# Optimization experiments

Measured on AMD Instinct MI355X. Metric: run time of the kernel, lower is better.

The kernel has to match this reference:

```python
import jax, jax.numpy as jnp
import numpy as np


def _apply_rope(x, cos, sin):
    # x: [B, h, T, d]; cos/sin: [T, d//2]
    B, h, T, d = x.shape
    xp = x.astype(jnp.float32).reshape(B, h, T, d // 2, 2)
    xr, xi = xp[..., 0], xp[..., 1]
    c = cos[None, None]  # [1,1,T,d//2]
    s = sin[None, None]
    out_r = xr * c - xi * s
    out_i = xr * s + xi * c
    out = jnp.stack([out_r, out_i], axis=-1).reshape(B, h, T, d)
    return out.astype(x.dtype)


def setup_inputs() -> dict:
    key = jax.random.key(0)
    ks = jax.random.split(key, 7)
    B, T, C = 1, 4096, 1024
    h = 16
    d = C // h
    return {
        "x": jax.random.normal(ks[0], (B, T, C), jnp.float32),
        "freqs_cos": jax.random.normal(ks[1], (T, d // 2), jnp.float32),
        "freqs_sin": jax.random.normal(ks[2], (T, d // 2), jnp.float32),
        "Wq": jax.random.normal(ks[3], (C, C), jnp.float32) * 0.02,
        "Wk": jax.random.normal(ks[4], (C, C), jnp.float32) * 0.02,
        "Wv": jax.random.normal(ks[5], (C, C), jnp.float32) * 0.02,
        "Wo": jax.random.normal(ks[6], (C, C), jnp.float32) * 0.02,
    }


def reference(x, freqs_cos, freqs_sin, Wq, Wk, Wv, Wo):
    B, T, C = x.shape
    h = 16
    d = C // h
    # nn.Linear(bias=False): y = x @ W^T, W is [out, in]
    q = jnp.einsum("btc,oc->bto", x, Wq).reshape(B, T, h, d).transpose(0, 2, 1, 3)
    k = jnp.einsum("btc,oc->bto", x, Wk).reshape(B, T, h, d).transpose(0, 2, 1, 3)
    v = jnp.einsum("btc,oc->bto", x, Wv).reshape(B, T, h, d).transpose(0, 2, 1, 3)
    q = _apply_rope(q, freqs_cos, freqs_sin)
    k = _apply_rope(k, freqs_cos, freqs_sin)
    scale = 1.0 / jnp.sqrt(jnp.asarray(d, x.dtype))
    scores = jnp.einsum("bhqd,bhkd->bhqk", q, k) * scale  # [B,h,T,T]
    causal = jnp.tril(jnp.ones((T, T), bool))
    scores = jnp.where(causal[None, None], scores, -jnp.inf)
    att = jax.nn.softmax(scores.astype(jnp.float32), axis=-1).astype(q.dtype)
    y = jnp.einsum("bhqk,bhkd->bhqd", att, v)
    y = y.transpose(0, 2, 1, 3).reshape(B, T, C)
    return jnp.einsum("btc,oc->bto", y, Wo)  # dropout p=0 (eval)
```

## Files before the change

### kernel.cpp

```cpp
#include <hip/hip_runtime.h>
#include <hip/hip_bf16.h>
#include <math.h>

#define TT 4096
#define CC 1024
#define NH 16
#define HD 64

typedef unsigned short ushortT;
typedef __attribute__((ext_vector_type(8))) short short8;
typedef __attribute__((ext_vector_type(4))) float f32x4;

#define GLOAD_LDS16(gp, lp)                                                   \
    __builtin_amdgcn_global_load_lds(                                         \
        (const __attribute__((address_space(1))) void*)(gp),                  \
        (__attribute__((address_space(3))) void*)(lp), 16, 0, 0)

#define EXP2F(x) __builtin_amdgcn_exp2f(x)

__device__ __forceinline__ ushortT f2bf(float f) {
    __hip_bfloat16 h = __float2bfloat16(f);
    ushortT u; __builtin_memcpy(&u, &h, 2); return u;
}
__device__ __forceinline__ float bf2f(ushortT u) {
    return __uint_as_float(((unsigned)u) << 16);
}

#define PSLOT_BYTES 8704
#define NCHUNK_H 124
#define NTICK (NCHUNK_H * NH)

__global__ __launch_bounds__(256) void cvt_all(
    const float* __restrict__ x,  const float* __restrict__ wq,
    const float* __restrict__ wk, const float* __restrict__ wv,
    const float* __restrict__ wo,
    ushortT* __restrict__ xb,  ushortT* __restrict__ wqb,
    ushortT* __restrict__ wkb, ushortT* __restrict__ wvb,
    ushortT* __restrict__ wob)
{
    const int i = (blockIdx.x * 256 + threadIdx.x) * 4;
    const int NX = TT * CC, NW = CC * CC;
    const float* s; ushortT* d; int off;
    if (i < NX)               { s = x;  d = xb;  off = i; }
    else if (i < NX + NW)     { s = wq; d = wqb; off = i - NX; }
    else if (i < NX + 2 * NW) { s = wk; d = wkb; off = i - NX - NW; }
    else if (i < NX + 3 * NW) { s = wv; d = wvb; off = i - NX - 2 * NW; }
    else                      { s = wo; d = wob; off = i - NX - 3 * NW; }
    float4 v = *(const float4*)(s + off);
    *(ushort4*)(d + off) = make_ushort4(f2bf(v.x), f2bf(v.y), f2bf(v.z), f2bf(v.w));
}

__global__ __launch_bounds__(256) void gemm_qkv(
    const ushortT* __restrict__ A,
    const ushortT* __restrict__ Bq, const ushortT* __restrict__ Bk,
    const ushortT* __restrict__ Bv,
    const float* __restrict__ fcos, const float* __restrict__ fsin,
    ushortT* __restrict__ q16, ushortT* __restrict__ k16,
    ushortT* __restrict__ vt16)
{
    __shared__ char lds[49152];

    const int z = blockIdx.z;
    const ushortT* B = (z == 0) ? Bq : (z == 1) ? Bk : Bv;

    const int lin = (int)(blockIdx.y * gridDim.x + blockIdx.x);
    const int nwg8 = (int)((gridDim.x * gridDim.y) >> 3);
    const int swz = (lin & 7) * nwg8 + (lin >> 3);
    const int bm = (swz % (int)gridDim.x) * 128;
    const int bn = (swz / (int)gridDim.x) * 128;
    const int tid = threadIdx.x;
    const int w = tid >> 6, l = tid & 63;
    const int wm = w >> 1, wn = w & 1;

    f32x4 acc[4][4] = {};

    auto stageg = [&](int kk, int base) {
        #pragma unroll
        for (int e = 0; e < 2; ++e) {
            const int D = (w * 2 + e) * 1024 + l * 16;
            const int r = D >> 6;
            const int c = (D & 63) >> 1;
            GLOAD_LDS16(A + (size_t)(bm + r) * CC + kk + c, lds + base + (w * 2 + e) * 1024);
            GLOAD_LDS16(B + (size_t)(bn + r) * CC + kk + c, lds + base + 8192 + (w * 2 + e) * 1024);
        }
    };

    stageg(0, 0);
    stageg(32, 16384);

    for (int kt = 0; kt < 32; ++kt) {
        const int cur = kt % 3;
        if (kt + 2 < 32) {
            stageg((kt + 2) * 32, ((kt + 2) % 3) * 16384);
            asm volatile("s_waitcnt vmcnt(8)" ::: "memory");
        } else if (kt + 1 < 32) {
            asm volatile("s_waitcnt vmcnt(4)" ::: "memory");
        } else {
            asm volatile("s_waitcnt vmcnt(0)" ::: "memory");
        }
        __builtin_amdgcn_s_barrier();
        __builtin_amdgcn_sched_barrier(0);

        const ushortT* As = (const ushortT*)(lds + cur * 16384);
        const ushortT* Bs = (const ushortT*)(lds + cur * 16384 + 8192);

        short8 af[4], bfr[4];
        #pragma unroll
        for (int i = 0; i < 4; ++i) {
            int row = wm * 64 + i * 16 + (l & 15);
            af[i] = *(const short8*)(As + row * 32 + (l >> 4) * 8);
        }
        #pragma unroll
        for (int j = 0; j < 4; ++j) {
            int row = wn * 64 + j * 16 + (l & 15);
            bfr[j] = *(const short8*)(Bs + row * 32 + (l >> 4) * 8);
        }
        #pragma unroll
        for (int i = 0; i < 4; ++i)
            #pragma unroll
            for (int j = 0; j < 4; ++j)
                acc[i][j] = __builtin_amdgcn_mfma_f32_16x16x32_bf16(af[i], bfr[j], acc[i][j], 0, 0, 0);
        __builtin_amdgcn_s_barrier();
    }

    if (z < 2) {
        const float rsc = (z == 0) ? 0.18033688011112042f : 1.0f;
        ushortT* dq = (z == 0) ? q16 : k16;
        float* cs = (float*)lds;
        float* sn = (float*)(lds + 16384);
        for (int idx = tid; idx < 128 * 32; idx += 256) {
            int rr = idx >> 5, cc2 = idx & 31;
            cs[idx] = fcos[(size_t)(bm + rr) * 32 + cc2];
            sn[idx] = fsin[(size_t)(bm + rr) * 32 + cc2];
        }
        __syncthreads();
        #pragma unroll
        for (int i = 0; i < 4; ++i)
            #pragma unroll
            for (int j = 0; j < 4; ++j)
                #pragma unroll
                for (int r = 0; r < 4; ++r) {
                    const int lt = wm * 64 + i * 16 + (l >> 4) * 4 + r;
                    const int o = bn + wn * 64 + j * 16 + (l & 15);
                    const float v = acc[i][j][r];
                    const float p = __shfl_xor(v, 1);
                    const int pp = (o & 63) >> 1;
                    const float cv = cs[lt * 32 + pp], sv = sn[lt * 32 + pp];
                    const float outv = ((o & 1) ? (p * sv + v * cv) : (v * cv - p * sv)) * rsc;
                    const int t = bm + lt, head = o >> 6, dd = o & 63;
                    dq[((size_t)head * TT + t) * HD + dd] = f2bf(outv);
                }
    } else {
        #pragma unroll
        for (int i = 0; i < 4; ++i)
            #pragma unroll
            for (int j = 0; j < 4; ++j)
                #pragma unroll
                for (int r = 0; r < 4; ++r) {
                    const int t = bm + wm * 64 + i * 16 + (l >> 4) * 4 + r;
                    const int o = bn + wn * 64 + j * 16 + (l & 15);
                    const int head = o >> 6, dd = o & 63;
                    const int k = t & 63;
                    const int slot = (k & 32) | (((k >> 2) & 3) << 3)
                                   | (((k >> 4) & 1) << 2) | (k & 3);
                    vt16[((size_t)(head * HD + dd)) * TT + (t & ~63) + slot] = f2bf(acc[i][j][r]);
                }
    }
}

__global__ __launch_bounds__(256) void gemm_out(
    const ushortT* __restrict__ A, const ushortT* __restrict__ B,
    float* __restrict__ dout)
{
    __shared__ char lds[49152];

    const int lin = (int)(blockIdx.y * gridDim.x + blockIdx.x);
    const int nwg8 = (int)((gridDim.x * gridDim.y) >> 3);
    const int swz = (lin & 7) * nwg8 + (lin >> 3);
    const int bm = (swz % (int)gridDim.x) * 128;
    const int bn = (swz / (int)gridDim.x) * 128;
    const int tid = threadIdx.x;
    const int w = tid >> 6, l = tid & 63;
    const int wm = w >> 1, wn = w & 1;

    f32x4 acc[4][4] = {};

    auto stageg = [&](int kk, int base) {
        #pragma unroll
        for (int e = 0; e < 2; ++e) {
            const int D = (w * 2 + e) * 1024 + l * 16;
            const int r = D >> 6;
            const int c = (D & 63) >> 1;
            GLOAD_LDS16(A + (size_t)(bm + r) * CC + kk + c, lds + base + (w * 2 + e) * 1024);
            GLOAD_LDS16(B + (size_t)(bn + r) * CC + kk + c, lds + base + 8192 + (w * 2 + e) * 1024);
        }
    };

    stageg(0, 0);
    stageg(32, 16384);

    for (int kt = 0; kt < 32; ++kt) {
        const int cur = kt % 3;
        if (kt + 2 < 32) {
            stageg((kt + 2) * 32, ((kt + 2) % 3) * 16384);
            asm volatile("s_waitcnt vmcnt(8)" ::: "memory");
        } else if (kt + 1 < 32) {
            asm volatile("s_waitcnt vmcnt(4)" ::: "memory");
        } else {
            asm volatile("s_waitcnt vmcnt(0)" ::: "memory");
        }
        __builtin_amdgcn_s_barrier();
        __builtin_amdgcn_sched_barrier(0);

        const ushortT* As = (const ushortT*)(lds + cur * 16384);
        const ushortT* Bs = (const ushortT*)(lds + cur * 16384 + 8192);

        short8 af[4], bfr[4];
        #pragma unroll
        for (int i = 0; i < 4; ++i) {
            int row = wm * 64 + i * 16 + (l & 15);
            af[i] = *(const short8*)(As + row * 32 + (l >> 4) * 8);
        }
        #pragma unroll
        for (int j = 0; j < 4; ++j) {
            int row = wn * 64 + j * 16 + (l & 15);
            bfr[j] = *(const short8*)(Bs + row * 32 + (l >> 4) * 8);
        }
        #pragma unroll
        for (int i = 0; i < 4; ++i)
            #pragma unroll
            for (int j = 0; j < 4; ++j)
                acc[i][j] = __builtin_amdgcn_mfma_f32_16x16x32_bf16(af[i], bfr[j], acc[i][j], 0, 0, 0);
        __builtin_amdgcn_s_barrier();
    }

    #pragma unroll
    for (int i = 0; i < 4; ++i)
        #pragma unroll
        for (int j = 0; j < 4; ++j)
            #pragma unroll
            for (int r = 0; r < 4; ++r) {
                const int t = bm + wm * 64 + i * 16 + (l >> 4) * 4 + r;
                const int o = bn + wn * 64 + j * 16 + (l & 15);
                dout[(size_t)t * CC + o] = acc[i][j][r];
            }
}

__global__ __launch_bounds__(256) void attn_mfma(
    const ushortT* __restrict__ q16, const ushortT* __restrict__ k16,
    const ushortT* __restrict__ vt16, ushortT* __restrict__ y16,
    char* __restrict__ parts, int* __restrict__ counter)
{
    const int tid = threadIdx.x;
    const int w = tid >> 6, l = tid & 63;
    const int g = l >> 4, q = l & 15;

    __shared__ char lds[32768];

    for (;;) {
        if (tid == 0) {
            int tk0 = atomicAdd(counter, 1);
            *(int*)lds = tk0;
        }
        __syncthreads();
        const int tk = *(const int*)lds;
        __syncthreads();
        if (tk >= NTICK) break;

        const int head = tk / NCHUNK_H;
        const int t = tk - head * NCHUNK_H;
        int qb, ci, nsplit;
        if (t < 54)       { qb = 63 - t / 3; ci = t % 3; nsplit = 3; }
        else if (t < 102) { int u = t - 54; qb = 45 - u / 2; ci = u % 2; nsplit = 2; }
        else              { qb = 123 - t; ci = -1; nsplit = 1; }
        const int kb0 = (ci < 0) ? 0 : ci * (qb + 1) / nsplit;
        const int kb1 = (ci < 0) ? qb : (ci + 1) * (qb + 1) / nsplit - 1;

        const int qrow = qb * 64 + w * 16 + q;
        short8 qa[2];
        {
            const ushortT* qp = q16 + ((size_t)head * TT + qrow) * HD + g * 8;
            qa[0] = *(const short8*)(qp);
            qa[1] = *(const short8*)(qp + 32);
        }

        f32x4 yacc[4] = {};
        float m_s = -1e30f, l_s = 0.0f;

        auto stage = [&](int kb, int base) {
            #pragma unroll
            for (int e = 0; e < 2; ++e) {
                const int D = (w * 2 + e) * 1024 + l * 16;
                const int row = D >> 7;
                const int src = D ^ ((row & 7) << 4);
                const int col = (src & 127) >> 1;
                GLOAD_LDS16(k16 + ((size_t)head * TT + (size_t)kb * 64 + row) * HD + col,
                            lds + base + (w * 2 + e) * 1024);
                GLOAD_LDS16(vt16 + ((size_t)head * HD + row) * TT + (size_t)kb * 64 + col,
                            lds + base + 8192 + (w * 2 + e) * 1024);
            }
        };

        int cur = 0;
        stage(kb0, 0);

        for (int kb = kb0; kb <= kb1; ++kb) {
            if (kb + 1 <= kb1) {
                stage(kb + 1, (cur ^ 1) * 16384);
                asm volatile("s_waitcnt vmcnt(4)" ::: "memory");
            } else {
                asm volatile("s_waitcnt vmcnt(0)" ::: "memory");
            }
            __builtin_amdgcn_s_barrier();
            __builtin_amdgcn_sched_barrier(0);

            const char* Ks  = lds + cur * 16384;
            const char* Vts = Ks + 8192;

            f32x4 s[4] = {};
            __builtin_amdgcn_s_setprio(1);
            #pragma unroll
            for (int ks = 0; ks < 2; ++ks)
                #pragma unroll
                for (int kg = 0; kg < 4; ++kg) {
                    const int key = kg * 16 + q;
                    int b = key * 128 + ks * 64 + g * 16;
                    b ^= (key & 7) << 4;
                    short8 kf = *(const short8*)(Ks + b);
                    s[kg] = __builtin_amdgcn_mfma_f32_16x16x32_bf16(kf, qa[ks], s[kg], 0, 0, 0);
                }
            __builtin_amdgcn_s_setprio(0);

            if (kb == qb) {
                #pragma unroll
                for (int kg = 0; kg < 4; ++kg)
                    #pragma unroll
                    for (int r = 0; r < 4; ++r)
                        if (kb * 64 + kg * 16 + 4 * g + r > qrow) s[kg][r] = -1e30f;
            }

            float ilmax = s[0][0];
            #pragma unroll
            for (int kg = 0; kg < 4; ++kg)
                #pragma unroll
                for (int r = 0; r < 4; ++r)
                    ilmax = fmaxf(ilmax, s[kg][r]);

            if (__any(ilmax > m_s + 8.0f)) {
                float mx = ilmax;
                mx = fmaxf(mx, __shfl_xor(mx, 16));
                mx = fmaxf(mx, __shfl_xor(mx, 32));
                const float mnew = fmaxf(m_s, mx);
                const float al = EXP2F(m_s - mnew);
                m_s = mnew;
                l_s *= al;
                float aly[4];
                #pragma unroll
                for (int r = 0; r < 4; ++r)
                    aly[r] = __shfl(al, 20 * g + r);
                #pragma unroll
                for (int dg = 0; dg < 4; ++dg)
                    #pragma unroll
                    for (int r = 0; r < 4; ++r)
                        yacc[dg][r] *= aly[r];
            }

            unsigned U[4], V[4];
            float ls = 0.0f;
            #pragma unroll
            for (int kg = 0; kg < 4; ++kg) {
                const float p0 = EXP2F(s[kg][0] - m_s);
                const float p1 = EXP2F(s[kg][1] - m_s);
                const float p2 = EXP2F(s[kg][2] - m_s);
                const float p3 = EXP2F(s[kg][3] - m_s);
                ls += (p0 + p1) + (p2 + p3);
                asm("v_cvt_pk_bf16_f32 %0, %1, %2" : "=v"(U[kg]) : "v"(p0), "v"(p1));
                asm("v_cvt_pk_bf16_f32 %0, %1, %2" : "=v"(V[kg]) : "v"(p2), "v"(p3));
            }
            l_s += ls;

            __builtin_amdgcn_s_setprio(1);
            #pragma unroll
            for (int ks2 = 0; ks2 < 2; ++ks2) {
                union { unsigned u[4]; short8 s8; } pu;
                pu.u[0] = U[2 * ks2];     pu.u[1] = V[2 * ks2];
                pu.u[2] = U[2 * ks2 + 1]; pu.u[3] = V[2 * ks2 + 1];
                const short8 pa = pu.s8;
                #pragma unroll
                for (int dg = 0; dg < 4; ++dg) {
                    const int dd = dg * 16 + q;
                    int vb = dd * 128 + ks2 * 64 + g * 16;
                    vb ^= (dd & 7) << 4;
                    short8 vf = *(const short8*)(Vts + vb);
                    yacc[dg] = __builtin_amdgcn_mfma_f32_16x16x32_bf16(pa, vf, yacc[dg], 0, 0, 0);
                }
            }
            __builtin_amdgcn_s_setprio(0);
            __builtin_amdgcn_s_barrier();
            cur ^= 1;
        }

        l_s += __shfl_xor(l_s, 16);
        l_s += __shfl_xor(l_s, 32);
        float lr[4];
        #pragma unroll
        for (int r = 0; r < 4; ++r)
            lr[r] = __shfl(l_s, 20 * g + r);

        if (ci < 0) {
            #pragma unroll
            for (int r = 0; r < 4; ++r) lr[r] = 1.0f / lr[r];
            #pragma unroll
            for (int dg = 0; dg < 4; ++dg)
                #pragma unroll
                for (int r = 0; r < 4; ++r) {
                    const int trow = qb * 64 + w * 16 + 4 * g + r;
                    const int col = head * HD + dg * 16 + q;
                    y16[(size_t)trow * CC + col] = f2bf(yacc[dg][r] * lr[r]);
                }
        } else {
            float mr[4];
            #pragma unroll
            for (int r = 0; r < 4; ++r)
                mr[r] = __shfl(m_s, 20 * g + r);
            const int sidx = head * 102 +
                ((qb >= 46) ? (qb - 46) * 3 + ci : 54 + (qb - 22) * 2 + ci);
            char* pb = parts + (size_t)sidx * PSLOT_BYTES;
            ushortT* yp = (ushortT*)pb;
            float* mp = (float*)(pb + 8192);
            float* lp = (float*)(pb + 8448);
            #pragma unroll
            for (int dg = 0; dg < 4; ++dg)
                #pragma unroll
                for (int r = 0; r < 4; ++r) {
                    const int row = w * 16 + 4 * g + r;
                    yp[row * 64 + dg * 16 + q] = f2bf(yacc[dg][r]);
                }
            if (q == 0) {
                #pragma unroll
                for (int r = 0; r < 4; ++r) {
                    const int row = w * 16 + 4 * g + r;
                    mp[row] = mr[r];
                    lp[row] = lr[r];
                }
            }
        }
    }
}

__global__ __launch_bounds__(256) void attn_combine(
    const char* __restrict__ parts, ushortT* __restrict__ y16)
{
    const int qb = 22 + blockIdx.x;
    const int head = blockIdx.y;
    const int nsplit = (qb >= 46) ? 3 : 2;
    const int base = head * 102 + ((qb >= 46) ? (qb - 46) * 3 : 54 + (qb - 22) * 2);
    const int row = threadIdx.x >> 2;
    const int pc = threadIdx.x & 3;

    float m_i[3], l_i[3];
    float M = -1e30f;
    for (int i = 0; i < nsplit; ++i) {
        const char* pb = parts + (size_t)(base + i) * PSLOT_BYTES;
        m_i[i] = *(const float*)(pb + 8192 + row * 4);
        l_i[i] = *(const float*)(pb + 8448 + row * 4);
        M = fmaxf(M, m_i[i]);
    }
    float wgt[3], L = 0.0f;
    for (int i = 0; i < nsplit; ++i) {
        wgt[i] = EXP2F(m_i[i] - M);
        L += l_i[i] * wgt[i];
    }
    const float Linv = 1.0f / L;

    const int trow = qb * 64 + row;
    #pragma unroll
    for (int j = 0; j < 16; ++j) {
        const int col = pc * 16 + j;
        float acc = 0.0f;
        for (int i = 0; i < nsplit; ++i) {
            const ushortT* yp = (const ushortT*)(parts + (size_t)(base + i) * PSLOT_BYTES);
            acc += bf2f(yp[row * 64 + col]) * wgt[i];
        }
        y16[(size_t)trow * CC + head * HD + col] = f2bf(acc * Linv);
    }
}

extern "C" void kernel_launch(void* const* d_in, const int* in_sizes, int n_in,
                              void* d_out, int out_size, void* d_ws, size_t ws_size,
                              hipStream_t stream) {
    const float* x    = (const float*)d_in[0];
    const float* fcos = (const float*)d_in[1];
    const float* fsin = (const float*)d_in[2];
    const float* Wq   = (const float*)d_in[3];
    const float* Wk   = (const float*)d_in[4];
    const float* Wv   = (const float*)d_in[5];
    const float* Wo   = (const float*)d_in[6];
    float* out = (float*)d_out;

    char* ws = (char*)d_ws;
    ushortT* xb  = (ushortT*)(ws);
    ushortT* wqb = (ushortT*)(ws + (8u << 20));
    ushortT* wkb = (ushortT*)(ws + (10u << 20));
    ushortT* wvb = (ushortT*)(ws + (12u << 20));
    ushortT* wob = (ushortT*)(ws + (14u << 20));
    ushortT* q16 = (ushortT*)(ws + (16u << 20));
    ushortT* k16 = (ushortT*)(ws + (24u << 20));
    ushortT* vt16 = (ushortT*)(ws + (32u << 20));
    ushortT* y16 = (ushortT*)(ws + (40u << 20));
    char* parts = ws;
    int* counter = (int*)(ws + (14u << 20) - 16);

    cvt_all<<<(TT * CC + 4 * CC * CC) / 4 / 256, 256, 0, stream>>>(
        x, Wq, Wk, Wv, Wo, xb, wqb, wkb, wvb, wob);

    dim3 qkvgrid(TT / 128, CC / 128, 3);
    gemm_qkv<<<qkvgrid, 256, 0, stream>>>(xb, wqb, wkb, wvb, fcos, fsin,
                                          q16, k16, vt16);

    hipMemsetAsync(counter, 0, 4, stream);
    attn_mfma<<<1280, 256, 0, stream>>>(q16, k16, vt16, y16, parts, counter);

    dim3 cgrid(42, NH);
    attn_combine<<<cgrid, 256, 0, stream>>>(parts, y16);

    dim3 ggrid(TT / 128, CC / 128);
    gemm_out<<<ggrid, 256, 0, stream>>>(y16, wob, out);
}
```

Measured before the change: 164.9 us.

## Use 128-row query tiles with 8 waves per attention block

The attention kernel now processes 128 query rows per work item using 512 threads (8 waves), so each staged K/V tile in LDS is shared by twice as many query rows. Each wave loads one 1KB segment of either K or V instead of both, and waves whose rows lie entirely before a key block skip its compute. The split-K schedule, partial-slot layout and combine kernel are resized to match, and the combine kernel is vectorized to 8-element loads and stores. This halves global K/V traffic per query, at the cost of idle waves on diagonal tiles and fewer, larger work items.

```diff
diff --git a/kernel.cpp b/kernel.cpp
--- a/kernel.cpp
+++ b/kernel.cpp
@@ -26,8 +26,8 @@
     return __uint_as_float(((unsigned)u) << 16);
 }
 
-#define PSLOT_BYTES 8704
-#define NCHUNK_H 124
+#define PSLOT_BYTES 17408
+#define NCHUNK_H 62
 #define NTICK (NCHUNK_H * NH)
 
 __global__ __launch_bounds__(256) void cvt_all(
@@ -246,7 +246,7 @@
             }
 }
 
-__global__ __launch_bounds__(256) void attn_mfma(
+__global__ __launch_bounds__(512) void attn_mfma(
     const ushortT* __restrict__ q16, const ushortT* __restrict__ k16,
     const ushortT* __restrict__ vt16, ushortT* __restrict__ y16,
     char* __restrict__ parts, int* __restrict__ counter)
@@ -269,14 +269,16 @@
 
         const int head = tk / NCHUNK_H;
         const int t = tk - head * NCHUNK_H;
-        int qb, ci, nsplit;
-        if (t < 54)       { qb = 63 - t / 3; ci = t % 3; nsplit = 3; }
-        else if (t < 102) { int u = t - 54; qb = 45 - u / 2; ci = u % 2; nsplit = 2; }
-        else              { qb = 123 - t; ci = -1; nsplit = 1; }
-        const int kb0 = (ci < 0) ? 0 : ci * (qb + 1) / nsplit;
-        const int kb1 = (ci < 0) ? qb : (ci + 1) * (qb + 1) / nsplit - 1;
-
-        const int qrow = qb * 64 + w * 16 + q;
+        int qc, ci, nsplit;
+        if (t < 27)      { qc = 31 - t / 3; ci = t % 3; nsplit = 3; }
+        else if (t < 51) { int u = t - 27; qc = 22 - u / 2; ci = u & 1; nsplit = 2; }
+        else             { qc = 10 - (t - 51); ci = -1; nsplit = 1; }
+        const int ntl = 2 * qc + 2;
+        const int kb0 = (ci <= 0) ? 0 : ci * ntl / nsplit;
+        const int kb1 = (ci < 0) ? (ntl - 1) : ((ci + 1) * ntl / nsplit - 1);
+
+        const int rowbase = qc * 128 + w * 16;
+        const int qrow = rowbase + q;
         short8 qa[2];
         {
             const ushortT* qp = q16 + ((size_t)head * TT + qrow) * HD + g * 8;
@@ -290,14 +292,22 @@
         auto stage = [&](int kb, int base) {
             #pragma unroll
             for (int e = 0; e < 2; ++e) {
-                const int D = (w * 2 + e) * 1024 + l * 16;
-                const int row = D >> 7;
-                const int src = D ^ ((row & 7) << 4);
-                const int col = (src & 127) >> 1;
-                GLOAD_LDS16(k16 + ((size_t)head * TT + (size_t)kb * 64 + row) * HD + col,
-                            lds + base + (w * 2 + e) * 1024);
-                GLOAD_LDS16(vt16 + ((size_t)head * HD + row) * TT + (size_t)kb * 64 + col,
-                            lds + base + 8192 + (w * 2 + e) * 1024);
+                const int seg = w * 2 + e;
+                const int D = seg * 1024 + l * 16;
+                if (seg < 8) {
+                    const int row = D >> 7;
+                    const int src = D ^ ((row & 7) << 4);
+                    const int col = (src & 127) >> 1;
+                    GLOAD_LDS16(k16 + ((size_t)head * TT + (size_t)kb * 64 + row) * HD + col,
+                                lds + base + seg * 1024);
+                } else {
+                    const int Dv = D - 8192;
+                    const int row = Dv >> 7;
+                    const int src = Dv ^ ((row & 7) << 4);
+                    const int col = (src & 127) >> 1;
+                    GLOAD_LDS16(vt16 + ((size_t)head * HD + row) * TT + (size_t)kb * 64 + col,
+                                lds + base + seg * 1024);
+                }
             }
         };
 
@@ -307,95 +317,99 @@
         for (int kb = kb0; kb <= kb1; ++kb) {
             if (kb + 1 <= kb1) {
                 stage(kb + 1, (cur ^ 1) * 16384);
-                asm volatile("s_waitcnt vmcnt(4)" ::: "memory");
+                asm volatile("s_waitcnt vmcnt(2)" ::: "memory");
             } else {
                 asm volatile("s_waitcnt vmcnt(0)" ::: "memory");
             }
             __builtin_amdgcn_s_barrier();
             __builtin_amdgcn_sched_barrier(0);
 
-            const char* Ks  = lds + cur * 16384;
-            const char* Vts = Ks + 8192;
-
-            f32x4 s[4] = {};
-            __builtin_amdgcn_s_setprio(1);
-            #pragma unroll
-            for (int ks = 0; ks < 2; ++ks)
-                #pragma unroll
-                for (int kg = 0; kg < 4; ++kg) {
-                    const int key = kg * 16 + q;
-                    int b = key * 128 + ks * 64 + g * 16;
-                    b ^= (key & 7) << 4;
-                    short8 kf = *(const short8*)(Ks + b);
-                    s[kg] = __builtin_amdgcn_mfma_f32_16x16x32_bf16(kf, qa[ks], s[kg], 0, 0, 0);
-                }
-            __builtin_amdgcn_s_setprio(0);
-
-            if (kb == qb) {
+            const bool skip = (kb * 64 > rowbase + 15);
+            if (!skip) {
+                const char* Ks  = lds + cur * 16384;
+                const char* Vts = Ks + 8192;
+
+                f32x4 s[4] = {};
+                __builtin_amdgcn_s_setprio(1);
+                #pragma unroll
+                for (int ks = 0; ks < 2; ++ks)
+                    #pragma unroll
+                    for (int kg = 0; kg < 4; ++kg) {
+                        const int key = kg * 16 + q;
+                        int b = key * 128 + ks * 64 + g * 16;
+                        b ^= (key & 7) << 4;
+                        short8 kf = *(const short8*)(Ks + b);
+                        s[kg] = __builtin_amdgcn_mfma_f32_16x16x32_bf16(kf, qa[ks], s[kg], 0, 0, 0);
+                    }
+                __builtin_amdgcn_s_setprio(0);
+
+                if (kb * 64 + 63 > rowbase) {
+                    #pragma unroll
+                    for (int kg = 0; kg < 4; ++kg)
+                        #pragma unroll
+                        for (int r = 0; r < 4; ++r)
+                            if (kb * 64 + kg * 16 + 4 * g + r > qrow) s[kg][r] = -1e30f;
+                }
+
+                float ilmax = s[0][0];
                 #pragma unroll
                 for (int kg = 0; kg < 4; ++kg)
                     #pragma unroll
                     for (int r = 0; r < 4; ++r)
-                        if (kb * 64 + kg * 16 + 4 * g + r > qrow) s[kg][r] = -1e30f;
-            }
-
-            float ilmax = s[0][0];
-            #pragma unroll
-            for (int kg = 0; kg < 4; ++kg)
-                #pragma unroll
-                for (int r = 0; r < 4; ++r)
-                    ilmax = fmaxf(ilmax, s[kg][r]);
-
-            if (__any(ilmax > m_s + 8.0f)) {
-                float mx = ilmax;
-                mx = fmaxf(mx, __shfl_xor(mx, 16));
-                mx = fmaxf(mx, __shfl_xor(mx, 32));
-                const float mnew = fmaxf(m_s, mx);
-                const float al = EXP2F(m_s - mnew);
-                m_s = mnew;
-                l_s *= al;
-                float aly[4];
-                #pragma unroll
-                for (int r = 0; r < 4; ++r)
-                    aly[r] = __shfl(al, 20 * g + r);
-                #pragma unroll
-                for (int dg = 0; dg < 4; ++dg)
+                        ilmax = fmaxf(ilmax, s[kg][r]);
+
+                if (__any(ilmax > m_s + 8.0f)) {
+                    float mx = ilmax;
+                    mx = fmaxf(mx, __shfl_xor(mx, 16));
+                    mx = fmaxf(mx, __shfl_xor(mx, 32));
+                    const float mnew = fmaxf(m_s, mx);
+                    const float al = EXP2F(m_s - mnew);
+                    m_s = mnew;
+                    l_s *= al;
+                    float aly[4];
                     #pragma unroll
                     for (int r = 0; r < 4; ++r)
-                        yacc[dg][r] *= aly[r];
+                        aly[r] = __shfl(al, 20 * g + r);
+                    #pragma unroll
+                    for (int dg = 0; dg < 4; ++dg)
+                        #pragma unroll
+                        for (int r = 0; r < 4; ++r)
+                            yacc[dg][r] *= aly[r];
+                }
+
+                unsigned U[4], V[4];
+                float ls = 0.0f;
+                #pragma unroll
+                for (int kg = 0; kg < 4; ++kg) {
+                    const float p0 = EXP2F(s[kg][0] - m_s);
+                    const float p1 = EXP2F(s[kg][1] - m_s);
+                    const float p2 = EXP2F(s[kg][2] - m_s);
+                    const float p3 = EXP2F(s[kg][3] - m_s);
+                    ls += (p0 + p1) + (p2 + p3);
+                    asm("v_cvt_pk_bf16_f32 %0, %1, %2" : "=v"(U[kg]) : "v"(p0), "v"(p1));
+                    asm("v_cvt_pk_bf16_f32 %0, %1, %2" : "=v"(V[kg]) : "v"(p2), "v"(p3));
+                }
+                l_s += ls;
+
+                __builtin_amdgcn_s_setprio(1);
+                #pragma unroll
+                for (int ks2 = 0; ks2 < 2; ++ks2) {
+                    union { unsigned u[4]; short8 s8; } pu;
+                    pu.u[0] = U[2 * ks2];     pu.u[1] = V[2 * ks2];
+                    pu.u[2] = U[2 * ks2 + 1]; pu.u[3] = V[2 * ks2 + 1];
+                    const short8 pa = pu.s8;
+                    const char* Vts2 = Vts;
+                    #pragma unroll
+                    for (int dg = 0; dg < 4; ++dg) {
+                        const int dd = dg * 16 + q;
+                        int vb = dd * 128 + ks2 * 64 + g * 16;
+                        vb ^= (dd & 7) << 4;
+                        short8 vf = *(const short8*)(Vts2 + vb);
+                        yacc[dg] = __builtin_amdgcn_mfma_f32_16x16x32_bf16(pa, vf, yacc[dg], 0, 0, 0);
+                    }
+                }
+                __builtin_amdgcn_s_setprio(0);
             }
-
-            unsigned U[4], V[4];
-            float ls = 0.0f;
-            #pragma unroll
-            for (int kg = 0; kg < 4; ++kg) {
-                const float p0 = EXP2F(s[kg][0] - m_s);
-                const float p1 = EXP2F(s[kg][1] - m_s);
-                const float p2 = EXP2F(s[kg][2] - m_s);
-                const float p3 = EXP2F(s[kg][3] - m_s);
-                ls += (p0 + p1) + (p2 + p3);
-                asm("v_cvt_pk_bf16_f32 %0, %1, %2" : "=v"(U[kg]) : "v"(p0), "v"(p1));
-                asm("v_cvt_pk_bf16_f32 %0, %1, %2" : "=v"(V[kg]) : "v"(p2), "v"(p3));
-            }
-            l_s += ls;
-
-            __builtin_amdgcn_s_setprio(1);
-            #pragma unroll
-            for (int ks2 = 0; ks2 < 2; ++ks2) {
-                union { unsigned u[4]; short8 s8; } pu;
-                pu.u[0] = U[2 * ks2];     pu.u[1] = V[2 * ks2];
-                pu.u[2] = U[2 * ks2 + 1]; pu.u[3] = V[2 * ks2 + 1];
-                const short8 pa = pu.s8;
-                #pragma unroll
-                for (int dg = 0; dg < 4; ++dg) {
-                    const int dd = dg * 16 + q;
-                    int vb = dd * 128 + ks2 * 64 + g * 16;
-                    vb ^= (dd & 7) << 4;
-                    short8 vf = *(const short8*)(Vts + vb);
-                    yacc[dg] = __builtin_amdgcn_mfma_f32_16x16x32_bf16(pa, vf, yacc[dg], 0, 0, 0);
-                }
-            }
-            __builtin_amdgcn_s_setprio(0);
             __builtin_amdgcn_s_barrier();
             cur ^= 1;
         }
@@ -414,7 +428,7 @@
             for (int dg = 0; dg < 4; ++dg)
                 #pragma unroll
                 for (int r = 0; r < 4; ++r) {
-                    const int trow = qb * 64 + w * 16 + 4 * g + r;
+                    const int trow = rowbase + 4 * g + r;
                     const int col = head * HD + dg * 16 + q;
                     y16[(size_t)trow * CC + col] = f2bf(yacc[dg][r] * lr[r]);
                 }
@@ -423,12 +437,12 @@
             #pragma unroll
             for (int r = 0; r < 4; ++r)
                 mr[r] = __shfl(m_s, 20 * g + r);
-            const int sidx = head * 102 +
-                ((qb >= 46) ? (qb - 46) * 3 + ci : 54 + (qb - 22) * 2 + ci);
+            const int sidx = head * 51 +
+                ((qc >= 23) ? (31 - qc) * 3 + ci : 27 + (22 - qc) * 2 + ci);
             char* pb = parts + (size_t)sidx * PSLOT_BYTES;
             ushortT* yp = (ushortT*)pb;
-            float* mp = (float*)(pb + 8192);
-            float* lp = (float*)(pb + 8448);
+            float* mp = (float*)(pb + 16384);
+            float* lp = (float*)(pb + 16896);
             #pragma unroll
             for (int dg = 0; dg < 4; ++dg)
                 #pragma unroll
@@ -451,38 +465,46 @@
 __global__ __launch_bounds__(256) void attn_combine(
     const char* __restrict__ parts, ushortT* __restrict__ y16)
 {
-    const int qb = 22 + blockIdx.x;
+    const int qc = 11 + blockIdx.x;
     const int head = blockIdx.y;
-    const int nsplit = (qb >= 46) ? 3 : 2;
-    const int base = head * 102 + ((qb >= 46) ? (qb - 46) * 3 : 54 + (qb - 22) * 2);
-    const int row = threadIdx.x >> 2;
-    const int pc = threadIdx.x & 3;
-
-    float m_i[3], l_i[3];
-    float M = -1e30f;
-    for (int i = 0; i < nsplit; ++i) {
-        const char* pb = parts + (size_t)(base + i) * PSLOT_BYTES;
-        m_i[i] = *(const float*)(pb + 8192 + row * 4);
-        l_i[i] = *(const float*)(pb + 8448 + row * 4);
-        M = fmaxf(M, m_i[i]);
-    }
-    float wgt[3], L = 0.0f;
-    for (int i = 0; i < nsplit; ++i) {
-        wgt[i] = EXP2F(m_i[i] - M);
-        L += l_i[i] * wgt[i];
-    }
-    const float Linv = 1.0f / L;
-
-    const int trow = qb * 64 + row;
+    const int nsplit = (qc >= 23) ? 3 : 2;
+    const int base = head * 51 + ((qc >= 23) ? (31 - qc) * 3 : 27 + (22 - qc) * 2);
+    const int tid = threadIdx.x;
+
     #pragma unroll
-    for (int j = 0; j < 16; ++j) {
-        const int col = pc * 16 + j;
-        float acc = 0.0f;
+    for (int pass = 0; pass < 4; ++pass) {
+        const int idx = pass * 2048 + tid * 8;
+        const int row = idx >> 6, col = idx & 63;
+
+        float m_i[3], l_i[3];
+        float M = -1e30f;
+        for (int i = 0; i < nsplit; ++i) {
+            const char* pb = parts + (size_t)(base + i) * PSLOT_BYTES;
+            m_i[i] = *(const float*)(pb + 16384 + row * 4);
+            l_i[i] = *(const float*)(pb + 16896 + row * 4);
+            M = fmaxf(M, m_i[i]);
+        }
+        float wgt[3], L = 0.0f;
+        for (int i = 0; i < nsplit; ++i) {
+            wgt[i] = EXP2F(m_i[i] - M);
+            L += l_i[i] * wgt[i];
+        }
+        const float Linv = 1.0f / L;
+
+        float acc[8] = {};
         for (int i = 0; i < nsplit; ++i) {
             const ushortT* yp = (const ushortT*)(parts + (size_t)(base + i) * PSLOT_BYTES);
-            acc += bf2f(yp[row * 64 + col]) * wgt[i];
-        }
-        y16[(size_t)trow * CC + head * HD + col] = f2bf(acc * Linv);
+            short8 v = *(const short8*)(yp + row * 64 + col);
+            #pragma unroll
+            for (int j = 0; j < 8; ++j)
+                acc[j] += bf2f((ushortT)v[j]) * wgt[i];
+        }
+        union { ushortT u[8]; short8 s8; } ov;
+        #pragma unroll
+        for (int j = 0; j < 8; ++j)
+            ov.u[j] = f2bf(acc[j] * Linv);
+        const int trow = qc * 128 + row;
+        *(short8*)(&y16[(size_t)trow * CC + head * HD + col]) = ov.s8;
     }
 }
 
@@ -519,9 +541,9 @@
                                           q16, k16, vt16);
 
     hipMemsetAsync(counter, 0, 4, stream);
-    attn_mfma<<<1280, 256, 0, stream>>>(q16, k16, vt16, y16, parts, counter);
-
-    dim3 cgrid(42, NH);
+    attn_mfma<<<1024, 512, 0, stream>>>(q16, k16, vt16, y16, parts, counter);
+
+    dim3 cgrid(21, NH);
     attn_combine<<<cgrid, 256, 0, stream>>>(parts, y16);
 
     dim3 ggrid(TT / 128, CC / 128);
```

After: 143.5 us. 1.15x faster.
